# Optimization experiments

Hardware: AMD Instinct MI355X
Metric: run time of the kernel (lower is better)

Reference implementation:

```python
import jax, jax.numpy as jnp
import numpy as np

# Real spherical harmonics, l=2 (2l+1 = 5 components), standard normalization.
C_XY   = float(0.5  * np.sqrt(15.0 / np.pi))
C_Z2   = float(0.25 * np.sqrt(5.0  / np.pi))
C_X2Y2 = float(0.25 * np.sqrt(15.0 / np.pi))

N_NODES  = 50000
N_EDGES  = 1_600_000
HIDDEN   = 32
CHANNELS = 16


def _sph_harm_l2(u):
    # u: [E,3] unit vectors -> [E,5]
    x, y, z = u[..., 0], u[..., 1], u[..., 2]
    return jnp.stack([
        C_XY * x * y,
        C_XY * y * z,
        C_Z2 * (3.0 * z * z - 1.0),
        C_XY * x * z,
        C_X2Y2 * (x * x - y * y),
    ], axis=-1)


def setup_inputs() -> dict:
    key = jax.random.key(0)
    k = jax.random.split(key, 6)
    positions = jax.random.normal(k[0], (N_NODES, 3), dtype=jnp.float32) * 10.0
    edge_index = jax.random.randint(k[1], (2, N_EDGES), 0, N_NODES)
    # radial MLP: dist [E,1] -> relu -> [E,CHANNELS]
    W1 = jax.random.normal(k[2], (1, HIDDEN), dtype=jnp.float32)
    b1 = jax.random.normal(k[3], (HIDDEN,), dtype=jnp.float32) * 0.1
    W2 = jax.random.normal(k[4], (HIDDEN, CHANNELS), dtype=jnp.float32) / np.sqrt(HIDDEN)
    b2 = jax.random.normal(k[5], (CHANNELS,), dtype=jnp.float32) * 0.1
    return {"positions": positions, "W1": W1, "b1": b1, "W2": W2, "b2": b2,
            "edge_index": edge_index}


def reference(positions, W1, b1, W2, b2, edge_index):
    i_arr = edge_index[0]
    j_arr = edge_index[1]
    # per-edge relative vectors + distances (point_cloud.getVectors / getDistance)
    rel = positions[i_arr] - positions[j_arr]            # [E,3]
    dist = jnp.linalg.norm(rel, axis=-1, keepdims=True)  # [E,1]
    dist = jnp.maximum(dist, 1e-8)                       # guard degenerate edges
    unit = rel / dist                                    # normalized vectors
    sh = _sph_harm_l2(unit)                              # [E,5] spharm(l_filter)
    # calculateRadialValues: radial MLP on distances -> [E,CHANNELS]
    h = jax.nn.relu(dist @ W1 + b1)
    radial = h @ W2 + b2
    # filter = spherical harmonics broadcast * per-channel radial values
    return radial[:, :, None] * sh[:, None, :]           # [E,CHANNELS,5]
```

## Files before the change

### kernel.cpp

```cpp
#include <hip/hip_runtime.h>
#include <math.h>

#define E_CNT 1600000
#define HID 32
#define CH 16
#define NSEG 33
#define TABF (8 * NSEG * 4)
#define TILE 320
#define GRID (E_CNT / TILE)
#define RSTR 17
#define SSTR 7

#define C_XY   1.0925484305920792f
#define C_Z2   0.31539156525252005f
#define C_X2Y2 0.5462742152960396f

__global__ void precompute_kernel(const float* __restrict__ W1,
                                  const float* __restrict__ b1,
                                  const float* __restrict__ W2,
                                  const float* __restrict__ b2,
                                  float* __restrict__ ws) {
    __shared__ float s_v[HID], s_w1[HID], s_b1[HID];
    __shared__ int s_rank[HID];
    int tid = threadIdx.x;
    if (tid < HID) {
        float w = W1[tid], b = b1[tid];
        float v = 0.0f;
        if (w != 0.0f) v = fmaxf(-b / w, 0.0f);
        s_v[tid] = v; s_w1[tid] = w; s_b1[tid] = b;
    }
    __syncthreads();
    if (tid < HID) {
        float v = s_v[tid];
        int r = 0;
        for (int k = 0; k < HID; ++k) {
            float vk = s_v[k];
            r += (vk < v || (vk == v && k < tid)) ? 1 : 0;
        }
        s_rank[tid] = r;
        ws[tid] = v;
    }
    __syncthreads();
    if (tid < NSEG * CH) {
        int m = tid / CH;
        int c = tid % CH;
        float A = 0.0f, B = b2[c];
        for (int k = 0; k < HID; ++k) {
            float w = s_w1[k], b = s_b1[k];
            bool act;
            if (w > 0.0f)      act = (s_rank[k] < m);
            else if (w < 0.0f) act = (s_rank[k] >= m);
            else               act = (b > 0.0f);
            if (act) {
                float w2 = W2[k * CH + c];
                A = fmaf(w, w2, A);
                B = fmaf(b, w2, B);
            }
        }
        const int q = c >> 2, xc = c & 3;
        ws[32 + (q * NSEG + m) * 4 + xc]       = A;
        ws[32 + ((q + 4) * NSEG + m) * 4 + xc] = B;
    }
}

__global__ __launch_bounds__(TILE) void edge_kernel(const float* __restrict__ pos,
                                                    const int* __restrict__ ei,
                                                    const float* __restrict__ ws,
                                                    float* __restrict__ out) {
    __shared__ __align__(16) float sTab[TABF];
    __shared__ float sR[TILE * RSTR];
    __shared__ float sSH[TILE * SSTR];

    const int t = threadIdx.x;
    const int e = blockIdx.x * TILE + t;

    const int ni = ei[e];
    const int nj = ei[E_CNT + e];

    for (int q = t; q < TABF; q += TILE) sTab[q] = ws[32 + q];

    float vbp[HID];
#pragma unroll
    for (int k = 0; k < HID; ++k) vbp[k] = ws[k];

    const float* pi = pos + 3 * ni;
    const float* pj = pos + 3 * nj;
    const float rx = pi[0] - pj[0];
    const float ry = pi[1] - pj[1];
    const float rz = pi[2] - pj[2];

    const float d2   = fmaf(rx, rx, fmaf(ry, ry, rz * rz));
    const float dist = fmaxf(sqrtf(d2), 1e-8f);
    const float inv  = __builtin_amdgcn_rcpf(dist);
    const float x = rx * inv, y = ry * inv, z = rz * inv;
    sSH[t * SSTR + 0] = C_XY * x * y;
    sSH[t * SSTR + 1] = C_XY * y * z;
    sSH[t * SSTR + 2] = C_Z2 * fmaf(3.0f * z, z, -1.0f);
    sSH[t * SSTR + 3] = C_XY * x * z;
    sSH[t * SSTR + 4] = C_X2Y2 * (x * x - y * y);

    int m = 0;
#pragma unroll
    for (int k = 0; k < HID; ++k) m += (vbp[k] < dist) ? 1 : 0;

    __syncthreads();

    {
        const float4* T4 = reinterpret_cast<const float4*>(sTab);
#pragma unroll
        for (int q = 0; q < 4; ++q) {
            const float4 a  = T4[q * NSEG + m];
            const float4 bb = T4[(q + 4) * NSEG + m];
            sR[t * RSTR + 4 * q + 0] = fmaf(dist, a.x, bb.x);
            sR[t * RSTR + 4 * q + 1] = fmaf(dist, a.y, bb.y);
            sR[t * RSTR + 4 * q + 2] = fmaf(dist, a.z, bb.z);
            sR[t * RSTR + 4 * q + 3] = fmaf(dist, a.w, bb.w);
        }
    }
    __syncthreads();

    const int w20 = t % 20;
    const int e0  = t / 20;
    const int p   = 4 * w20;
    const int ri0 =  p      / 5, si0 =  p      - 5 * ri0;
    const int ri1 = (p + 1) / 5, si1 = (p + 1) - 5 * ri1;
    const int ri2 = (p + 2) / 5, si2 = (p + 2) - 5 * ri2;
    const int ri3 = (p + 3) / 5, si3 = (p + 3) - 5 * ri3;
    const float* rb = &sR[e0 * RSTR];
    const float* sb = &sSH[e0 * SSTR];
    float4* ob = reinterpret_cast<float4*>(out) + (size_t)blockIdx.x * (TILE * 20) + t;
#pragma unroll
    for (int it = 0; it < 20; ++it) {
        const int ro = it * 16 * RSTR;
        const int so = it * 16 * SSTR;
        float4 o;
        o.x = rb[ro + ri0] * sb[so + si0];
        o.y = rb[ro + ri1] * sb[so + si1];
        o.z = rb[ro + ri2] * sb[so + si2];
        o.w = rb[ro + ri3] * sb[so + si3];
        ob[it * TILE] = o;
    }
}

extern "C" void kernel_launch(void* const* d_in, const int* in_sizes, int n_in,
                              void* d_out, int out_size, void* d_ws, size_t ws_size,
                              hipStream_t stream) {
    const float* pos = (const float*)d_in[0];
    const float* W1  = (const float*)d_in[1];
    const float* b1  = (const float*)d_in[2];
    const float* W2  = (const float*)d_in[3];
    const float* b2  = (const float*)d_in[4];
    const int*   ei  = (const int*)d_in[5];
    float* out = (float*)d_out;
    float* ws  = (float*)d_ws;

    precompute_kernel<<<1, 544, 0, stream>>>(W1, b1, W2, b2, ws);
    edge_kernel<<<GRID, TILE, 0, stream>>>(pos, ei, ws, out);
}
```

Baseline: 118.2 us.

## Fuse radial evaluation into output loop and use nontemporal stores

The per-edge radial-table step and its extra barrier are removed. Each output thread now looks up the table and computes the at most two radial values it needs, using per-edge distance and segment index stored in shared memory. The table layout becomes channel-major, the tile shrinks to 256 threads with an occupancy hint, and output writes use nontemporal stores to avoid polluting the cache. The cost is more index arithmetic and shared-memory reads per output vector, traded for less shared memory, one fewer sync and higher occupancy on this write-bound kernel.

```diff
diff --git a/kernel.cpp b/kernel.cpp
--- a/kernel.cpp
+++ b/kernel.cpp
@@ -5,15 +5,16 @@
 #define HID 32
 #define CH 16
 #define NSEG 33
-#define TABF (8 * NSEG * 4)
-#define TILE 320
+#define TABF (2 * CH * NSEG)
+#define TILE 256
 #define GRID (E_CNT / TILE)
-#define RSTR 17
-#define SSTR 7
+#define ESTR 9
 
 #define C_XY   1.0925484305920792f
 #define C_Z2   0.31539156525252005f
 #define C_X2Y2 0.5462742152960396f
+
+typedef float f32x4 __attribute__((ext_vector_type(4)));
 
 __global__ void precompute_kernel(const float* __restrict__ W1,
                                   const float* __restrict__ b1,
@@ -57,19 +58,17 @@
                 B = fmaf(b, w2, B);
             }
         }
-        const int q = c >> 2, xc = c & 3;
-        ws[32 + (q * NSEG + m) * 4 + xc]       = A;
-        ws[32 + ((q + 4) * NSEG + m) * 4 + xc] = B;
+        ws[32 + c * NSEG + m]             = A;
+        ws[32 + CH * NSEG + c * NSEG + m] = B;
     }
 }
 
-__global__ __launch_bounds__(TILE) void edge_kernel(const float* __restrict__ pos,
-                                                    const int* __restrict__ ei,
-                                                    const float* __restrict__ ws,
-                                                    float* __restrict__ out) {
-    __shared__ __align__(16) float sTab[TABF];
-    __shared__ float sR[TILE * RSTR];
-    __shared__ float sSH[TILE * SSTR];
+__global__ __launch_bounds__(TILE, 8) void edge_kernel(const float* __restrict__ pos,
+                                                       const int* __restrict__ ei,
+                                                       const float* __restrict__ ws,
+                                                       float* __restrict__ out) {
+    __shared__ float sTab[TABF];
+    __shared__ float sE[TILE * ESTR];
 
     const int t = threadIdx.x;
     const int e = blockIdx.x * TILE + t;
@@ -93,52 +92,48 @@
     const float dist = fmaxf(sqrtf(d2), 1e-8f);
     const float inv  = __builtin_amdgcn_rcpf(dist);
     const float x = rx * inv, y = ry * inv, z = rz * inv;
-    sSH[t * SSTR + 0] = C_XY * x * y;
-    sSH[t * SSTR + 1] = C_XY * y * z;
-    sSH[t * SSTR + 2] = C_Z2 * fmaf(3.0f * z, z, -1.0f);
-    sSH[t * SSTR + 3] = C_XY * x * z;
-    sSH[t * SSTR + 4] = C_X2Y2 * (x * x - y * y);
+
+    float* row_w = &sE[t * ESTR];
+    row_w[0] = C_XY * x * y;
+    row_w[1] = C_XY * y * z;
+    row_w[2] = C_Z2 * fmaf(3.0f * z, z, -1.0f);
+    row_w[3] = C_XY * x * z;
+    row_w[4] = C_X2Y2 * (x * x - y * y);
+    row_w[5] = dist;
 
     int m = 0;
 #pragma unroll
     for (int k = 0; k < HID; ++k) m += (vbp[k] < dist) ? 1 : 0;
+    row_w[6] = __int_as_float(m);
 
     __syncthreads();
 
-    {
-        const float4* T4 = reinterpret_cast<const float4*>(sTab);
-#pragma unroll
-        for (int q = 0; q < 4; ++q) {
-            const float4 a  = T4[q * NSEG + m];
-            const float4 bb = T4[(q + 4) * NSEG + m];
-            sR[t * RSTR + 4 * q + 0] = fmaf(dist, a.x, bb.x);
-            sR[t * RSTR + 4 * q + 1] = fmaf(dist, a.y, bb.y);
-            sR[t * RSTR + 4 * q + 2] = fmaf(dist, a.z, bb.z);
-            sR[t * RSTR + 4 * q + 3] = fmaf(dist, a.w, bb.w);
-        }
-    }
-    __syncthreads();
-
-    const int w20 = t % 20;
-    const int e0  = t / 20;
-    const int p   = 4 * w20;
-    const int ri0 =  p      / 5, si0 =  p      - 5 * ri0;
-    const int ri1 = (p + 1) / 5, si1 = (p + 1) - 5 * ri1;
-    const int ri2 = (p + 2) / 5, si2 = (p + 2) - 5 * ri2;
-    const int ri3 = (p + 3) / 5, si3 = (p + 3) - 5 * ri3;
-    const float* rb = &sR[e0 * RSTR];
-    const float* sb = &sSH[e0 * SSTR];
-    float4* ob = reinterpret_cast<float4*>(out) + (size_t)blockIdx.x * (TILE * 20) + t;
+    f32x4* ob = reinterpret_cast<f32x4*>(out) + (size_t)blockIdx.x * (TILE * 20) + t;
 #pragma unroll
     for (int it = 0; it < 20; ++it) {
-        const int ro = it * 16 * RSTR;
-        const int so = it * 16 * SSTR;
-        float4 o;
-        o.x = rb[ro + ri0] * sb[so + si0];
-        o.y = rb[ro + ri1] * sb[so + si1];
-        o.z = rb[ro + ri2] * sb[so + si2];
-        o.w = rb[ro + ri3] * sb[so + si3];
-        ob[it * TILE] = o;
+        const int idx4 = t + TILE * it;
+        const int el = idx4 / 20;
+        const int u  = idx4 - el * 20;
+        const int p  = 4 * u;
+        const int rA  =  p      / 5;
+        const int ri1 = (p + 1) / 5;
+        const int ri2 = (p + 2) / 5;
+        const int rB  = (p + 3) / 5;
+        const int si0 =  p      - 5 * rA;
+        const int si1 = (p + 1) - 5 * ri1;
+        const int si2 = (p + 2) - 5 * ri2;
+        const int si3 = (p + 3) - 5 * rB;
+        const float* row = &sE[el * ESTR];
+        const float d = row[5];
+        const int   mm = __float_as_int(row[6]);
+        const float rvA = fmaf(d, sTab[rA * NSEG + mm], sTab[CH * NSEG + rA * NSEG + mm]);
+        const float rvB = fmaf(d, sTab[rB * NSEG + mm], sTab[CH * NSEG + rB * NSEG + mm]);
+        f32x4 o;
+        o.x = rvA * row[si0];
+        o.y = (ri1 == rA ? rvA : rvB) * row[si1];
+        o.z = (ri2 == rA ? rvA : rvB) * row[si2];
+        o.w = rvB * row[si3];
+        __builtin_nontemporal_store(o, ob + it * TILE);
     }
 }
 
```

Measured after the change: 113.3 us. 4.2% less time.
